# Kernel tuning notes

Measured on AMD Instinct MI355X. Metric: run time of the kernel, lower is better.

The kernel has to match this reference:

```python
import jax, jax.numpy as jnp
import numpy as np

N, E, G = 100_000, 1_600_000, 256
F_IN, H, C = 28, 4, 64
NEG_SLOPE = 0.2
LN_EPS = 1e-5


def _layernorm(x, w, b):
    mu = jnp.mean(x, axis=-1, keepdims=True)
    var = jnp.mean((x - mu) ** 2, axis=-1, keepdims=True)
    return (x - mu) * jax.lax.rsqrt(var + LN_EPS) * w + b


def _gat(x, W, a_src, a_dst, bias, src, dst):
    # PyG GATConv: heads=H, concat=False (mean over heads), add_self_loops=True
    n = x.shape[0]
    loop = jnp.arange(n, dtype=src.dtype)
    s = jnp.concatenate([src, loop])
    d = jnp.concatenate([dst, loop])
    xh = jnp.einsum('nf,hfc->nhc', x, W)              # [N,H,C]
    al_s = jnp.einsum('nhc,hc->nh', xh, a_src)        # [N,H]
    al_d = jnp.einsum('nhc,hc->nh', xh, a_dst)
    e = jax.nn.leaky_relu(al_s[s] + al_d[d], NEG_SLOPE)   # [E',H]
    m = jax.ops.segment_max(e, d, num_segments=n)
    ex = jnp.exp(e - m[d])
    den = jax.ops.segment_sum(ex, d, num_segments=n)
    w = ex / den[d]                                    # scatter-softmax over dst
    out = jax.ops.segment_sum(xh[s] * w[:, :, None], d, num_segments=n)  # [N,H,C]
    return jnp.mean(out, axis=1) + bias


def _gin(x, w1, b1, w2, b2, src, dst):
    # GINConv, eps=0: mlp((1+0)*x + sum_{j->i} x_j)
    agg = jax.ops.segment_sum(x[src], dst, num_segments=x.shape[0])
    h = jax.nn.relu((x + agg) @ w1 + b1)
    return h @ w2 + b2


def _global_attention(x, gw1, gb1, gw2, gb2, batch):
    gate = jax.nn.relu(x @ gw1 + gb1) @ gw2 + gb2      # [N,1]
    m = jax.ops.segment_max(gate, batch, num_segments=G)
    ex = jnp.exp(gate - m[batch])
    den = jax.ops.segment_sum(ex, batch, num_segments=G)
    a = ex / den[batch]
    return jax.ops.segment_sum(a * x, batch, num_segments=G)  # [G,C]


def setup_inputs() -> dict:
    key = jax.random.key(0)
    ks = jax.random.split(key, 32)
    rn = lambda k, shp, s=0.05: (jax.random.normal(k, shp, jnp.float32) * s)
    inp = {
        'x': rn(ks[0], (N, F_IN), 1.0),
        'src': jax.random.randint(ks[1], (E,), 0, N, jnp.int32),
        'dst': jax.random.randint(ks[2], (E,), 0, N, jnp.int32),
        'batch': jnp.sort(jax.random.randint(ks[3], (N,), 0, G, jnp.int32)),
        # GAT layer 1
        'W1': rn(ks[4], (H, F_IN, C)), 'a1s': rn(ks[5], (H, C)), 'a1d': rn(ks[6], (H, C)), 'bg1': jnp.zeros((C,), jnp.float32),
        # GIN mlp1
        'm1w1': rn(ks[7], (C, C)), 'm1b1': jnp.zeros((C,), jnp.float32), 'm1w2': rn(ks[8], (C, C)), 'm1b2': jnp.zeros((C,), jnp.float32),
        'ln1w': jnp.ones((C,), jnp.float32), 'ln1b': jnp.zeros((C,), jnp.float32),
        # GAT layer 2
        'W2': rn(ks[9], (H, C, C)), 'a2s': rn(ks[10], (H, C)), 'a2d': rn(ks[11], (H, C)), 'bg2': jnp.zeros((C,), jnp.float32),
        # GIN mlp2
        'm2w1': rn(ks[12], (C, C)), 'm2b1': jnp.zeros((C,), jnp.float32), 'm2w2': rn(ks[13], (C, C)), 'm2b2': jnp.zeros((C,), jnp.float32),
        'ln2w': jnp.ones((C,), jnp.float32), 'ln2b': jnp.zeros((C,), jnp.float32),
        # gate_nn
        'gw1': rn(ks[14], (C, C)), 'gb1': jnp.zeros((C,), jnp.float32), 'gw2': rn(ks[15], (C, 1)), 'gb2': jnp.zeros((1,), jnp.float32),
        # head
        'l1w': rn(ks[16], (C, 2 * C)), 'l1b': jnp.zeros((2 * C,), jnp.float32),
        'lnfw': jnp.ones((2 * C,), jnp.float32), 'lnfb': jnp.zeros((2 * C,), jnp.float32),
        'l2w': rn(ks[17], (2 * C, 6)), 'l2b': jnp.zeros((6,), jnp.float32),
    }
    return inp


def reference(x, src, dst, batch, W1, a1s, a1d, bg1, m1w1, m1b1, m1w2, m1b2, ln1w, ln1b,
              W2, a2s, a2d, bg2, m2w1, m2b1, m2w2, m2b2, ln2w, ln2b,
              gw1, gb1, gw2, gb2, l1w, l1b, lnfw, lnfb, l2w, l2b):
    # dropout is identity at inference
    xg1 = jax.nn.relu(_gat(x, W1, a1s, a1d, bg1, src, dst))
    x1 = _layernorm(xg1 + _gin(xg1, m1w1, m1b1, m1w2, m1b2, src, dst), ln1w, ln1b)
    xg2 = jax.nn.relu(_gat(x1, W2, a2s, a2d, bg2, src, dst))
    x2 = _layernorm(xg2 + _gin(xg2, m2w1, m2b1, m2w2, m2b2, src, dst), ln2w, ln2b)
    xg = _global_attention(x2, gw1, gb1, gw2, gb2, batch)
    xg = jax.nn.relu(_layernorm(xg @ l1w + l1b, lnfw, lnfb))
    return xg @ l2w + l2b  # [G, 6]
```

## Files before the change

kernel.cpp:

```cpp
#include <hip/hip_runtime.h>

#define N_N 100000
#define N_E 1600000
#define N_G 256
#define F_IN 28
#define HEADS 4
#define CH 64
#define NEG 0.2f
#define LN_EPS 1e-5f

typedef __attribute__((ext_vector_type(8))) short short8v;
typedef __attribute__((ext_vector_type(4))) float float4v;

__device__ __forceinline__ float lrelu(float x) { return x > 0.f ? x : NEG * x; }

__device__ __forceinline__ float wsum(float v) {
#pragma unroll
  for (int o = 32; o > 0; o >>= 1) v += __shfl_xor(v, o, 64);
  return v;
}
__device__ __forceinline__ float wmax(float v) {
#pragma unroll
  for (int o = 32; o > 0; o >>= 1) v = fmaxf(v, __shfl_xor(v, o, 64));
  return v;
}
__device__ __forceinline__ int wsumi(int v) {
#pragma unroll
  for (int o = 32; o > 0; o >>= 1) v += __shfl_xor(v, o, 64);
  return v;
}

__device__ __forceinline__ float bfs(unsigned short u) {
  return __uint_as_float((unsigned)u << 16);
}
__device__ __forceinline__ unsigned short f2bf(float v) {
  unsigned u = __float_as_uint(v);
  return (unsigned short)((u + 0x7fff + ((u >> 16) & 1)) >> 16);
}

__global__ __launch_bounds__(256) void k_deg(const int* __restrict__ dst, int* deg) {
  int e = blockIdx.x * 256 + threadIdx.x;
  if (e < N_E) atomicAdd(&deg[dst[e]], 1);
}

__global__ __launch_bounds__(256) void k_bsum(const int* __restrict__ deg, int* __restrict__ bsum) {
  __shared__ int l[4];
  int t = threadIdx.x;
  int i = blockIdx.x * 256 + t;
  int v = (i < N_N) ? deg[i] : 0;
  int s = wsumi(v);
  if ((t & 63) == 0) l[t >> 6] = s;
  __syncthreads();
  if (t == 0) bsum[blockIdx.x] = l[0] + l[1] + l[2] + l[3];
}

__global__ __launch_bounds__(512) void k_scanb(const int* __restrict__ bsum, int* __restrict__ bofs, int nb) {
  __shared__ int l[512];
  int t = threadIdx.x;
  int v = (t < nb) ? bsum[t] : 0;
  l[t] = v;
  __syncthreads();
  for (int o = 1; o < 512; o <<= 1) {
    int a = (t >= o) ? l[t - o] : 0;
    __syncthreads();
    l[t] += a;
    __syncthreads();
  }
  if (t < nb) bofs[t] = l[t] - v;
}

__global__ __launch_bounds__(256) void k_indptr(const int* __restrict__ deg, const int* __restrict__ bofs,
                                                int* __restrict__ indptr, int* __restrict__ fill) {
  __shared__ int l[256];
  int t = threadIdx.x;
  int i = blockIdx.x * 256 + t;
  int v = (i < N_N) ? deg[i] : 0;
  l[t] = v;
  __syncthreads();
  for (int o = 1; o < 256; o <<= 1) {
    int a = (t >= o) ? l[t - o] : 0;
    __syncthreads();
    l[t] += a;
    __syncthreads();
  }
  if (i < N_N) {
    int p = bofs[blockIdx.x] + l[t] - v;
    indptr[i] = p;
    fill[i] = p;
  }
  if (i == 0) indptr[N_N] = N_E;
}

__global__ __launch_bounds__(256) void k_scatter(const int* __restrict__ src, const int* __restrict__ dst,
                                                 int* fill, int* __restrict__ csr) {
  int e = blockIdx.x * 256 + threadIdx.x;
  if (e < N_E) {
    int d = dst[e];
    int p = atomicAdd(&fill[d], 1);
    csr[p] = src[e];
  }
}

__global__ __launch_bounds__(256) void k_sortw(const int* __restrict__ indptr, int* __restrict__ csr) {
  int wv = threadIdx.x >> 6, lane = threadIdx.x & 63;
  int i = blockIdx.x * 4 + wv;
  if (i >= N_N) return;
  int b = indptr[i], e = indptr[i + 1];
  int deg = e - b;
  if (deg <= 1) return;
  if (deg <= 64) {
    int v = (lane < deg) ? csr[b + lane] : 0x7fffffff;
    int rank = 0;
    for (int j = 0; j < deg; ++j) {
      int vj = __shfl(v, j, 64);
      rank += ((vj < v) || (vj == v && j < lane)) ? 1 : 0;
    }
    if (lane < deg) csr[b + rank] = v;
  } else if (lane == 0) {
    for (int j = b + 1; j < e; ++j) {
      int key = csr[j];
      int k = j - 1;
      while (k >= b && csr[k] > key) { csr[k + 1] = csr[k]; --k; }
      csr[k + 1] = key;
    }
  }
}

__global__ __launch_bounds__(512) void k_gbounds(const int* __restrict__ batch, int* __restrict__ gptr) {
  int g = threadIdx.x;
  if (g > N_G) return;
  int lo = 0, hi = N_N;
  while (lo < hi) {
    int mid = (lo + hi) >> 1;
    if (batch[mid] < g) lo = mid + 1;
    else hi = mid;
  }
  gptr[g] = lo;
}

template <int F>
__global__ __launch_bounds__(256) void k_avec(const float* __restrict__ W, const float* __restrict__ as_,
                                              const float* __restrict__ ad_, float* __restrict__ wsv,
                                              float* __restrict__ wdv) {
  int idx = blockIdx.x * 256 + threadIdx.x;
  if (idx >= HEADS * F) return;
  int h = idx / F, f = idx % F;
  float s = 0.f, d = 0.f;
  for (int c = 0; c < 64; ++c) {
    float w = W[(h * F + f) * 64 + c];
    s = fmaf(w, as_[h * 64 + c], s);
    d = fmaf(w, ad_[h * 64 + c], d);
  }
  wsv[idx] = s;
  wdv[idx] = d;
}

template <int F>
__global__ __launch_bounds__(256) void k_al2(const float* __restrict__ xin, const float* __restrict__ wsv,
                                             const float* __restrict__ wdv, float* __restrict__ al_s,
                                             float* __restrict__ al_d) {
  constexpr int FP = (F % 2 == 0) ? F + 1 : F;
  __shared__ float xl[64][FP];
  __shared__ float wsl[HEADS][F], wdl[HEADS][F];
  int t = threadIdx.x;
  for (int idx = t; idx < HEADS * F; idx += 256) {
    wsl[idx / F][idx % F] = wsv[idx];
    wdl[idx / F][idx % F] = wdv[idx];
  }
  int base = blockIdx.x * 64;
  for (int idx = t; idx < 64 * F; idx += 256) {
    int n = idx / F, f = idx % F;
    int i = base + n;
    xl[n][f] = (i < N_N) ? xin[(size_t)i * F + f] : 0.f;
  }
  __syncthreads();
  int n = t >> 2, h = t & 3;
  int i = base + n;
  if (i < N_N) {
    float s = 0.f, d = 0.f;
#pragma unroll
    for (int f = 0; f < F; ++f) {
      float xv = xl[n][f];
      s = fmaf(xv, wsl[h][f], s);
      d = fmaf(xv, wdl[h][f], d);
    }
    al_s[i * 4 + h] = s;
    al_d[i * 4 + h] = d;
  }
}

template <int F, int NW>
__global__ __launch_bounds__(64 * NW, 4) void k_gat(const float* __restrict__ xin, const int* __restrict__ indptr,
                                                    const int* __restrict__ csr, const float* __restrict__ al_s,
                                                    const float* __restrict__ al_d, const float* __restrict__ W,
                                                    const float* __restrict__ bias, float* __restrict__ xg) {
  constexpr int K = HEADS * F;
  constexpr int KP = (K + 31) & ~31;
  constexpr int KROW = KP + 8;
  __shared__ unsigned short Bt[64][KROW];
  __shared__ unsigned short Ash[16][KROW];
  __shared__ int s_idx[NW][64];
  __shared__ float4 s_w[NW][64];
  int t = threadIdx.x;
  for (int idx = t; idx < K * 64; idx += 64 * NW) {
    int c = idx & 63, hf = idx >> 6;
    Bt[c][hf] = f2bf(W[(size_t)hf * 64 + c]);
  }
  if constexpr (KP > K) {
    for (int idx = t; idx < 64 * (KP - K); idx += 64 * NW)
      Bt[idx / (KP - K)][K + idx % (KP - K)] = 0;
    for (int idx = t; idx < 16 * (KP - K); idx += 64 * NW)
      Ash[idx / (KP - K)][K + idx % (KP - K)] = 0;
  }
  __syncthreads();
  int wv = t >> 6, lane = t & 63;
  int lanef = lane & 31;
  int half = lane >> 5;
  int l15 = lane & 15, g8 = (lane >> 4) * 8;
  float bias_c = (wv < 4) ? bias[16 * wv + l15] : 0.f;
  for (int base = blockIdx.x * 16; base < N_N; base += gridDim.x * 16) {
#pragma unroll
    for (int rep = 0; rep < 2; ++rep) {
      int i = base + wv * 2 + rep;
      if (i < N_N) {
        int b = indptr[i], e = indptr[i + 1];
        float4 ad4 = *(const float4*)&al_d[i * 4];
        float4 as4 = *(const float4*)&al_s[i * 4];
        float ws0 = __expf(lrelu(as4.x + ad4.x));
        float ws1 = __expf(lrelu(as4.y + ad4.y));
        float ws2 = __expf(lrelu(as4.z + ad4.z));
        float ws3 = __expf(lrelu(as4.w + ad4.w));
        float xself = (lane < F) ? xin[(size_t)i * F + lane] : 0.f;
        float a0 = ws0 * xself, a1 = ws1 * xself, a2 = ws2 * xself, a3 = ws3 * xself;
        if (F == F_IN && half) { a0 = 0.f; a1 = 0.f; a2 = 0.f; a3 = 0.f; }
        float pd0 = 0.f, pd1 = 0.f, pd2 = 0.f, pd3 = 0.f;
        for (int cb = b; cb < e; cb += 64) {
          int cnt = min(64, e - cb);
          bool act = (cb + lane) < e;
          int s = 0;
          float w0 = 0.f, w1 = 0.f, w2 = 0.f, w3 = 0.f;
          if (act) {
            s = csr[cb + lane];
            float4 a4 = *(const float4*)&al_s[s * 4];
            w0 = __expf(lrelu(a4.x + ad4.x));
            w1 = __expf(lrelu(a4.y + ad4.y));
            w2 = __expf(lrelu(a4.z + ad4.z));
            w3 = __expf(lrelu(a4.w + ad4.w));
          }
          pd0 += w0; pd1 += w1; pd2 += w2; pd3 += w3;
          s_idx[wv][lane] = s;
          s_w[wv][lane] = make_float4(w0, w1, w2, w3);
          if (F == F_IN) {
            for (int je = 0; je < cnt; je += 16) {
              int sj[8];
#pragma unroll
              for (int u = 0; u < 8; ++u) sj[u] = s_idx[wv][je + 2 * u + half];
              float xr[8];
#pragma unroll
              for (int u = 0; u < 8; ++u)
                xr[u] = (lanef < F_IN) ? xin[(size_t)sj[u] * F_IN + lanef] : 0.f;
#pragma unroll
              for (int u = 0; u < 8; ++u) {
                float4 w4 = s_w[wv][je + 2 * u + half];
                a0 = fmaf(w4.x, xr[u], a0);
                a1 = fmaf(w4.y, xr[u], a1);
                a2 = fmaf(w4.z, xr[u], a2);
                a3 = fmaf(w4.w, xr[u], a3);
              }
            }
          } else {
            for (int je = 0; je < cnt; je += 8) {
              int sj[8];
#pragma unroll
              for (int u = 0; u < 8; ++u) sj[u] = s_idx[wv][je + u];
              float xr[8];
#pragma unroll
              for (int u = 0; u < 8; ++u) xr[u] = xin[(size_t)sj[u] * F + lane];
#pragma unroll
              for (int u = 0; u < 8; ++u) {
                float4 w4 = s_w[wv][je + u];
                a0 = fmaf(w4.x, xr[u], a0);
                a1 = fmaf(w4.y, xr[u], a1);
                a2 = fmaf(w4.z, xr[u], a2);
                a3 = fmaf(w4.w, xr[u], a3);
              }
            }
          }
        }
        if (F == F_IN) {
          a0 += __shfl_xor(a0, 32, 64);
          a1 += __shfl_xor(a1, 32, 64);
          a2 += __shfl_xor(a2, 32, 64);
          a3 += __shfl_xor(a3, 32, 64);
        }
        float dn0 = wsum(pd0) + ws0;
        float dn1 = wsum(pd1) + ws1;
        float dn2 = wsum(pd2) + ws2;
        float dn3 = wsum(pd3) + ws3;
        a0 /= dn0; a1 /= dn1; a2 /= dn2; a3 /= dn3;
        if (lane < F) {
          int n = wv * 2 + rep;
          Ash[n][0 * F + lane] = f2bf(a0);
          Ash[n][1 * F + lane] = f2bf(a1);
          Ash[n][2 * F + lane] = f2bf(a2);
          Ash[n][3 * F + lane] = f2bf(a3);
        }
      }
    }
    __syncthreads();
    if (wv < 4) {
      float4v c4 = {0.f, 0.f, 0.f, 0.f};
#pragma unroll
      for (int kk = 0; kk < KP; kk += 32) {
        short8v af = *(const short8v*)&Ash[l15][kk + g8];
        short8v bf = *(const short8v*)&Bt[16 * wv + l15][kk + g8];
        c4 = __builtin_amdgcn_mfma_f32_16x16x32_bf16(af, bf, c4, 0, 0, 0);
      }
#pragma unroll
      for (int reg = 0; reg < 4; ++reg) {
        int node = base + (g8 >> 1) + reg;
        if (node < N_N) {
          float o = fmaxf(fmaf(c4[reg], 0.25f, bias_c), 0.f);
          xg[(size_t)node * 64 + 16 * wv + l15] = o;
        }
      }
    }
    __syncthreads();
  }
}

template <int NW, bool FUSE_AL, bool FUSE_GATE>
__global__ __launch_bounds__(64 * NW, 4) void k_gin(const int* __restrict__ indptr, const int* __restrict__ csr,
                                                    const float* __restrict__ xg,
                                                    const float* __restrict__ w1,
                                                    const float* __restrict__ b1, const float* __restrict__ w2,
                                                    const float* __restrict__ b2, const float* __restrict__ lnw,
                                                    const float* __restrict__ lnb,
                                                    float* __restrict__ xo,
                                                    const float* __restrict__ wsv, const float* __restrict__ wdv,
                                                    float* __restrict__ al_s, float* __restrict__ al_d,
                                                    const float* __restrict__ gw1, const float* __restrict__ gb1,
                                                    const float* __restrict__ gw2, const float* __restrict__ gb2,
                                                    float* __restrict__ gate) {
  constexpr int KR = 72;
  __shared__ unsigned short W1t[64][KR], W2t[64][KR];
  __shared__ unsigned short GW1t[FUSE_GATE ? 64 : 1][FUSE_GATE ? KR : 1];
  __shared__ unsigned short WVt[FUSE_AL ? 16 : 1][FUSE_AL ? KR : 1];
  __shared__ unsigned short A1h[16][KR], A1l[16][KR], A2s[16][KR];
  __shared__ float A3[16][68];
  __shared__ unsigned short A4[FUSE_GATE ? 16 : 1][FUSE_GATE ? KR : 1];
  __shared__ float gred[4][16];
  int t = threadIdx.x;
  for (int idx = t; idx < 4096; idx += 64 * NW) {
    int k = idx >> 6, c = idx & 63;
    W1t[c][k] = f2bf(w1[idx]);
    W2t[c][k] = f2bf(w2[idx]);
    if constexpr (FUSE_GATE) GW1t[c][k] = f2bf(gw1[idx]);
  }
  if constexpr (FUSE_AL) {
    for (int idx = t; idx < 16 * 64; idx += 64 * NW) {
      int j = idx >> 6, k = idx & 63;
      float v = (j < 4) ? wsv[j * 64 + k] : (j < 8 ? wdv[(j - 4) * 64 + k] : 0.f);
      WVt[j][k] = f2bf(v);
    }
  }
  __syncthreads();
  int wv = t >> 6, lane = t & 63;
  int l15 = lane & 15, g8 = (lane >> 4) * 8;
  float b1c = 0.f, b2c = 0.f, gb1c = 0.f, gw2c = 0.f;
  if (wv < 4) {
    b1c = b1[16 * wv + l15];
    b2c = b2[16 * wv + l15];
    if constexpr (FUSE_GATE) {
      gb1c = gb1[16 * wv + l15];
      gw2c = gw2[16 * wv + l15];
    }
  }
  float lnwv = lnw[lane], lnbv = lnb[lane];
  float gb2v = FUSE_GATE ? gb2[0] : 0.f;
  for (int base = blockIdx.x * 16; base < N_N; base += gridDim.x * 16) {
    float xis[2];
#pragma unroll
    for (int rep = 0; rep < 2; ++rep) {
      int i = base + wv * 2 + rep;
      if (i < N_N) {
        int b = indptr[i], e = indptr[i + 1];
        float xi = xg[(size_t)i * 64 + lane];
        xis[rep] = xi;
        float acc = xi;
        for (int j = b; j < e; j += 8) {
          int cj[8];
#pragma unroll
          for (int u = 0; u < 8; ++u) cj[u] = csr[min(j + u, e - 1)];
          float v[8];
#pragma unroll
          for (int u = 0; u < 8; ++u) v[u] = xg[(size_t)cj[u] * 64 + lane];
#pragma unroll
          for (int u = 0; u < 8; ++u) acc += (j + u) < e ? v[u] : 0.f;
        }
        int n = wv * 2 + rep;
        unsigned short hb = f2bf(acc);
        A1h[n][lane] = hb;
        A1l[n][lane] = f2bf(acc - bfs(hb));
      }
    }
    __syncthreads();
    if (wv < 4) {
      float4v c4 = {0.f, 0.f, 0.f, 0.f};
#pragma unroll
      for (int kk = 0; kk < 64; kk += 32) {
        short8v bf = *(const short8v*)&W1t[16 * wv + l15][kk + g8];
        short8v ah = *(const short8v*)&A1h[l15][kk + g8];
        c4 = __builtin_amdgcn_mfma_f32_16x16x32_bf16(ah, bf, c4, 0, 0, 0);
        short8v al = *(const short8v*)&A1l[l15][kk + g8];
        c4 = __builtin_amdgcn_mfma_f32_16x16x32_bf16(al, bf, c4, 0, 0, 0);
      }
#pragma unroll
      for (int reg = 0; reg < 4; ++reg)
        A2s[(g8 >> 1) + reg][16 * wv + l15] = f2bf(fmaxf(c4[reg] + b1c, 0.f));
    }
    __syncthreads();
    if (wv < 4) {
      float4v c4 = {0.f, 0.f, 0.f, 0.f};
#pragma unroll
      for (int kk = 0; kk < 64; kk += 32) {
        short8v af = *(const short8v*)&A2s[l15][kk + g8];
        short8v bf = *(const short8v*)&W2t[16 * wv + l15][kk + g8];
        c4 = __builtin_amdgcn_mfma_f32_16x16x32_bf16(af, bf, c4, 0, 0, 0);
      }
#pragma unroll
      for (int reg = 0; reg < 4; ++reg) A3[(g8 >> 1) + reg][16 * wv + l15] = c4[reg] + b2c;
    }
    __syncthreads();
#pragma unroll
    for (int rep = 0; rep < 2; ++rep) {
      int i = base + wv * 2 + rep;
      if (i < N_N) {
        int n = wv * 2 + rep;
        float res = xis[rep] + A3[n][lane];
        float mu = wsum(res) * (1.f / 64.f);
        float d = res - mu;
        float var = wsum(d * d) * (1.f / 64.f);
        float xov = fmaf(d * rsqrtf(var + LN_EPS), lnwv, lnbv);
        xo[(size_t)i * 64 + lane] = xov;
        if constexpr (FUSE_AL) {
          unsigned short hb = f2bf(xov);
          A1h[n][lane] = hb;
          A1l[n][lane] = f2bf(xov - bfs(hb));
        }
        if constexpr (FUSE_GATE) A4[n][lane] = f2bf(xov);
      }
    }
    if constexpr (FUSE_AL) {
      __syncthreads();
      if (wv == 0) {
        float4v c4 = {0.f, 0.f, 0.f, 0.f};
#pragma unroll
        for (int kk = 0; kk < 64; kk += 32) {
          short8v bf = *(const short8v*)&WVt[l15][kk + g8];
          short8v ah = *(const short8v*)&A1h[l15][kk + g8];
          c4 = __builtin_amdgcn_mfma_f32_16x16x32_bf16(ah, bf, c4, 0, 0, 0);
          short8v al = *(const short8v*)&A1l[l15][kk + g8];
          c4 = __builtin_amdgcn_mfma_f32_16x16x32_bf16(al, bf, c4, 0, 0, 0);
        }
#pragma unroll
        for (int reg = 0; reg < 4; ++reg) {
          int node = base + (g8 >> 1) + reg;
          if (node < N_N) {
            if (l15 < 4) al_s[node * 4 + l15] = c4[reg];
            else if (l15 < 8) al_d[node * 4 + (l15 - 4)] = c4[reg];
          }
        }
      }
      __syncthreads();
    }
    if constexpr (FUSE_GATE) {
      __syncthreads();
      if (wv < 4) {
        float4v c4 = {0.f, 0.f, 0.f, 0.f};
#pragma unroll
        for (int kk = 0; kk < 64; kk += 32) {
          short8v af = *(const short8v*)&A4[l15][kk + g8];
          short8v bf = *(const short8v*)&GW1t[16 * wv + l15][kk + g8];
          c4 = __builtin_amdgcn_mfma_f32_16x16x32_bf16(af, bf, c4, 0, 0, 0);
        }
#pragma unroll
        for (int reg = 0; reg < 4; ++reg) {
          float m = fmaxf(c4[reg] + gb1c, 0.f) * gw2c;
          m += __shfl_xor(m, 1, 64);
          m += __shfl_xor(m, 2, 64);
          m += __shfl_xor(m, 4, 64);
          m += __shfl_xor(m, 8, 64);
          if (l15 == 0) gred[wv][(g8 >> 1) + reg] = m;
        }
      }
      __syncthreads();
      if (wv == 0 && lane < 16) {
        int node = base + lane;
        if (node < N_N)
          gate[node] = gred[0][lane] + gred[1][lane] + gred[2][lane] + gred[3][lane] + gb2v;
      }
      __syncthreads();
    }
  }
}

__global__ __launch_bounds__(256) void k_pool(const int* __restrict__ gptr, const float* __restrict__ gate,
                                              const float* __restrict__ x2, float* __restrict__ pooled) {
  int g = blockIdx.x;
  int t = threadIdx.x, wv = t >> 6, lane = t & 63;
  __shared__ float red[256];
  int b = gptr[g], e = gptr[g + 1];
  if (b == e) {
    if (t < 64) pooled[g * 64 + t] = 0.f;
    return;
  }
  float m = -1e30f;
  for (int j = b + t; j < e; j += 256) m = fmaxf(m, gate[j]);
  m = wmax(m);
  if (lane == 0) red[wv] = m;
  __syncthreads();
  m = fmaxf(fmaxf(red[0], red[1]), fmaxf(red[2], red[3]));
  __syncthreads();
  float dn = 0.f;
  for (int j = b + t; j < e; j += 256) dn += __expf(gate[j] - m);
  dn = wsum(dn);
  if (lane == 0) red[wv] = dn;
  __syncthreads();
  dn = red[0] + red[1] + red[2] + red[3];
  __syncthreads();
  float acc = 0.f;
  for (int j = b + wv; j < e; j += 4) acc = fmaf(__expf(gate[j] - m), x2[(size_t)j * 64 + lane], acc);
  red[t] = acc;
  __syncthreads();
  if (t < 64) pooled[g * 64 + t] = (red[t] + red[t + 64] + red[t + 128] + red[t + 192]) / dn;
}

__global__ __launch_bounds__(128) void k_head(const float* __restrict__ pooled, const float* __restrict__ l1w,
                                              const float* __restrict__ l1b, const float* __restrict__ lnfw,
                                              const float* __restrict__ lnfb, const float* __restrict__ l2w,
                                              const float* __restrict__ l2b, float* __restrict__ out) {
  int g = blockIdx.x, t = threadIdx.x;
  __shared__ float pl[64], zl[128], red[2];
  if (t < 64) pl[t] = pooled[g * 64 + t];
  __syncthreads();
  float y = l1b[t];
#pragma unroll 8
  for (int k = 0; k < 64; ++k) y = fmaf(pl[k], l1w[k * 128 + t], y);
  int wv = t >> 6, lane = t & 63;
  float s = wsum(y);
  if (lane == 0) red[wv] = s;
  __syncthreads();
  float mu = (red[0] + red[1]) * (1.f / 128.f);
  float d = y - mu;
  __syncthreads();
  s = wsum(d * d);
  if (lane == 0) red[wv] = s;
  __syncthreads();
  float var = (red[0] + red[1]) * (1.f / 128.f);
  float z = fmaxf(fmaf(d * rsqrtf(var + LN_EPS), lnfw[t], lnfb[t]), 0.f);
  zl[t] = z;
  __syncthreads();
  if (t < 6) {
    float o = l2b[t];
    for (int k = 0; k < 128; ++k) o = fmaf(zl[k], l2w[k * 6 + t], o);
    out[g * 6 + t] = o;
  }
}

extern "C" void kernel_launch(void* const* d_in, const int* in_sizes, int n_in,
                              void* d_out, int out_size, void* d_ws, size_t ws_size,
                              hipStream_t stream) {
  const float* x = (const float*)d_in[0];
  const int* src = (const int*)d_in[1];
  const int* dst = (const int*)d_in[2];
  const int* batch = (const int*)d_in[3];
  const float* W1 = (const float*)d_in[4];
  const float* a1s = (const float*)d_in[5];
  const float* a1d = (const float*)d_in[6];
  const float* bg1 = (const float*)d_in[7];
  const float* m1w1 = (const float*)d_in[8];
  const float* m1b1 = (const float*)d_in[9];
  const float* m1w2 = (const float*)d_in[10];
  const float* m1b2 = (const float*)d_in[11];
  const float* ln1w = (const float*)d_in[12];
  const float* ln1b = (const float*)d_in[13];
  const float* W2 = (const float*)d_in[14];
  const float* a2s = (const float*)d_in[15];
  const float* a2d = (const float*)d_in[16];
  const float* bg2 = (const float*)d_in[17];
  const float* m2w1 = (const float*)d_in[18];
  const float* m2b1 = (const float*)d_in[19];
  const float* m2w2 = (const float*)d_in[20];
  const float* m2b2 = (const float*)d_in[21];
  const float* ln2w = (const float*)d_in[22];
  const float* ln2b = (const float*)d_in[23];
  const float* gw1 = (const float*)d_in[24];
  const float* gb1 = (const float*)d_in[25];
  const float* gw2 = (const float*)d_in[26];
  const float* gb2 = (const float*)d_in[27];
  const float* l1w = (const float*)d_in[28];
  const float* l1b = (const float*)d_in[29];
  const float* lnfw = (const float*)d_in[30];
  const float* lnfb = (const float*)d_in[31];
  const float* l2w = (const float*)d_in[32];
  const float* l2b = (const float*)d_in[33];
  float* out = (float*)d_out;

  char* ws = (char*)d_ws;
  size_t off = 0;
  auto alloc = [&](size_t bytes) -> void* {
    void* p = ws + off;
    off += (bytes + 255) & ~(size_t)255;
    return p;
  };
  int* indptr = (int*)alloc((N_N + 1) * sizeof(int));
  int* fill = (int*)alloc(N_N * sizeof(int));
  int* csr = (int*)alloc((size_t)N_E * sizeof(int));
  int* bsum = (int*)alloc(512 * sizeof(int));
  int* bofs = (int*)alloc(512 * sizeof(int));
  int* gptr = (int*)alloc(257 * sizeof(int));
  float* wsv = (float*)alloc(HEADS * 64 * sizeof(float));
  float* wdv = (float*)alloc(HEADS * 64 * sizeof(float));
  float* al_s = (float*)alloc((size_t)N_N * 4 * sizeof(float));
  float* al_d = (float*)alloc((size_t)N_N * 4 * sizeof(float));
  float* gate = (float*)alloc((size_t)N_N * sizeof(float));
  float* pooled = (float*)alloc(N_G * 64 * sizeof(float));
  float* xg = (float*)alloc((size_t)N_N * 64 * sizeof(float));
  float* xv = (float*)alloc((size_t)N_N * 64 * sizeof(float));
  (void)ws_size; (void)n_in; (void)in_sizes; (void)out_size;

  const int NBE = (N_E + 255) / 256;
  const int NBN = (N_N + 255) / 256;

  hipMemsetAsync(fill, 0, (size_t)N_N * sizeof(int), stream);
  k_deg<<<NBE, 256, 0, stream>>>(dst, fill);
  k_bsum<<<NBN, 256, 0, stream>>>(fill, bsum);
  k_scanb<<<1, 512, 0, stream>>>(bsum, bofs, NBN);
  k_indptr<<<NBN, 256, 0, stream>>>(fill, bofs, indptr, fill);
  k_scatter<<<NBE, 256, 0, stream>>>(src, dst, fill, csr);
  k_sortw<<<(N_N + 3) / 4, 256, 0, stream>>>(indptr, csr);
  k_gbounds<<<1, 512, 0, stream>>>(batch, gptr);

  k_avec<F_IN><<<1, 256, 0, stream>>>(W1, a1s, a1d, wsv, wdv);
  k_al2<F_IN><<<(N_N + 63) / 64, 256, 0, stream>>>(x, wsv, wdv, al_s, al_d);
  k_gat<F_IN, 8><<<2048, 512, 0, stream>>>(x, indptr, csr, al_s, al_d, W1, bg1, xg);
  k_avec<CH><<<1, 256, 0, stream>>>(W2, a2s, a2d, wsv, wdv);
  k_gin<8, true, false><<<2048, 512, 0, stream>>>(indptr, csr, xg, m1w1, m1b1, m1w2, m1b2, ln1w, ln1b,
                                                  xv, wsv, wdv, al_s, al_d, gw1, gb1, gw2, gb2, gate);
  k_gat<CH, 8><<<2048, 512, 0, stream>>>(xv, indptr, csr, al_s, al_d, W2, bg2, xg);
  k_gin<8, false, true><<<2048, 512, 0, stream>>>(indptr, csr, xg, m2w1, m2b1, m2w2, m2b2, ln2w, ln2b,
                                                  xv, wsv, wdv, al_s, al_d, gw1, gb1, gw2, gb2, gate);
  k_pool<<<N_G, 256, 0, stream>>>(gptr, gate, xv, pooled);
  k_head<<<N_G, 128, 0, stream>>>(pooled, l1w, l1b, lnfw, lnfb, l2w, l2b, out);
}
```

Baseline: 719.6 us.

## Build CSR via two-level bucketed sort using shared-memory histograms

New measurement: 622.4 us. 13.5% less time.

```diff
diff --git a/kernel.cpp b/kernel.cpp
--- a/kernel.cpp
+++ b/kernel.cpp
@@ -8,6 +8,8 @@
 #define CH 64
 #define NEG 0.2f
 #define LN_EPS 1e-5f
+#define NBKT 391
+#define BCAP 6144
 
 typedef __attribute__((ext_vector_type(8))) short short8v;
 typedef __attribute__((ext_vector_type(4))) float float4v;
@@ -22,11 +24,6 @@
 __device__ __forceinline__ float wmax(float v) {
 #pragma unroll
   for (int o = 32; o > 0; o >>= 1) v = fmaxf(v, __shfl_xor(v, o, 64));
-  return v;
-}
-__device__ __forceinline__ int wsumi(int v) {
-#pragma unroll
-  for (int o = 32; o > 0; o >>= 1) v += __shfl_xor(v, o, 64);
   return v;
 }
 
@@ -38,26 +35,25 @@
   return (unsigned short)((u + 0x7fff + ((u >> 16) & 1)) >> 16);
 }
 
-__global__ __launch_bounds__(256) void k_deg(const int* __restrict__ dst, int* deg) {
-  int e = blockIdx.x * 256 + threadIdx.x;
-  if (e < N_E) atomicAdd(&deg[dst[e]], 1);
-}
-
-__global__ __launch_bounds__(256) void k_bsum(const int* __restrict__ deg, int* __restrict__ bsum) {
-  __shared__ int l[4];
+
+__global__ __launch_bounds__(256) void k_ccount(const int* __restrict__ dst, int* __restrict__ ccnt) {
+  __shared__ int h[NBKT];
   int t = threadIdx.x;
-  int i = blockIdx.x * 256 + t;
-  int v = (i < N_N) ? deg[i] : 0;
-  int s = wsumi(v);
-  if ((t & 63) == 0) l[t >> 6] = s;
-  __syncthreads();
-  if (t == 0) bsum[blockIdx.x] = l[0] + l[1] + l[2] + l[3];
-}
-
-__global__ __launch_bounds__(512) void k_scanb(const int* __restrict__ bsum, int* __restrict__ bofs, int nb) {
+  for (int i = t; i < NBKT; i += 256) h[i] = 0;
+  __syncthreads();
+  int base = blockIdx.x * 4096;
+  int cnt = min(4096, N_E - base);
+  for (int j = t; j < cnt; j += 256) atomicAdd(&h[dst[base + j] >> 8], 1);
+  __syncthreads();
+  for (int i = t; i < NBKT; i += 256)
+    if (h[i]) atomicAdd(&ccnt[i], h[i]);
+}
+
+__global__ __launch_bounds__(512) void k_cscan(const int* __restrict__ ccnt, int* __restrict__ cbase,
+                                               int* __restrict__ cfill) {
   __shared__ int l[512];
   int t = threadIdx.x;
-  int v = (t < nb) ? bsum[t] : 0;
+  int v = (t < NBKT) ? ccnt[t] : 0;
   l[t] = v;
   __syncthreads();
   for (int o = 1; o < 512; o <<= 1) {
@@ -66,62 +62,142 @@
     l[t] += a;
     __syncthreads();
   }
-  if (t < nb) bofs[t] = l[t] - v;
-}
-
-__global__ __launch_bounds__(256) void k_indptr(const int* __restrict__ deg, const int* __restrict__ bofs,
-                                                int* __restrict__ indptr, int* __restrict__ fill) {
-  __shared__ int l[256];
+  if (t < NBKT) {
+    cbase[t] = l[t] - v;
+    cfill[t] = l[t] - v;
+  }
+}
+
+__global__ __launch_bounds__(256) void k_cscat(const int* __restrict__ src, const int* __restrict__ dst,
+                                               int* cfill, unsigned long long* __restrict__ pairs) {
+  __shared__ unsigned long long pl[4096];
+  __shared__ unsigned long long outp[4096];
+  __shared__ int h[NBKT], sc[NBKT], gpos[NBKT], f2[NBKT];
   int t = threadIdx.x;
-  int i = blockIdx.x * 256 + t;
-  int v = (i < N_N) ? deg[i] : 0;
-  l[t] = v;
-  __syncthreads();
-  for (int o = 1; o < 256; o <<= 1) {
-    int a = (t >= o) ? l[t - o] : 0;
-    __syncthreads();
-    l[t] += a;
-    __syncthreads();
-  }
-  if (i < N_N) {
-    int p = bofs[blockIdx.x] + l[t] - v;
-    indptr[i] = p;
-    fill[i] = p;
-  }
-  if (i == 0) indptr[N_N] = N_E;
-}
-
-__global__ __launch_bounds__(256) void k_scatter(const int* __restrict__ src, const int* __restrict__ dst,
-                                                 int* fill, int* __restrict__ csr) {
-  int e = blockIdx.x * 256 + threadIdx.x;
-  if (e < N_E) {
-    int d = dst[e];
-    int p = atomicAdd(&fill[d], 1);
-    csr[p] = src[e];
-  }
-}
-
-__global__ __launch_bounds__(256) void k_sortw(const int* __restrict__ indptr, int* __restrict__ csr) {
-  int wv = threadIdx.x >> 6, lane = threadIdx.x & 63;
-  int i = blockIdx.x * 4 + wv;
-  if (i >= N_N) return;
-  int b = indptr[i], e = indptr[i + 1];
-  int deg = e - b;
-  if (deg <= 1) return;
-  if (deg <= 64) {
-    int v = (lane < deg) ? csr[b + lane] : 0x7fffffff;
-    int rank = 0;
-    for (int j = 0; j < deg; ++j) {
-      int vj = __shfl(v, j, 64);
-      rank += ((vj < v) || (vj == v && j < lane)) ? 1 : 0;
-    }
-    if (lane < deg) csr[b + rank] = v;
-  } else if (lane == 0) {
-    for (int j = b + 1; j < e; ++j) {
-      int key = csr[j];
-      int k = j - 1;
-      while (k >= b && csr[k] > key) { csr[k + 1] = csr[k]; --k; }
-      csr[k + 1] = key;
+  for (int i = t; i < NBKT; i += 256) {
+    h[i] = 0;
+    f2[i] = 0;
+  }
+  __syncthreads();
+  int base = blockIdx.x * 4096;
+  int cnt = min(4096, N_E - base);
+  for (int j = t; j < cnt; j += 256) {
+    int d = dst[base + j];
+    pl[j] = ((unsigned long long)(unsigned)d << 32) | (unsigned)src[base + j];
+    atomicAdd(&h[d >> 8], 1);
+  }
+  __syncthreads();
+  for (int i = t; i < NBKT; i += 256) sc[i] = h[i];
+  __syncthreads();
+  for (int o = 1; o < NBKT; o <<= 1) {
+    int v0 = 0, v1 = 0;
+    int i2 = t + 256;
+    if (t >= o) v0 = sc[t - o];
+    if (i2 < NBKT && i2 >= o) v1 = sc[i2 - o];
+    __syncthreads();
+    if (t >= o) sc[t] += v0;
+    if (i2 < NBKT && i2 >= o) sc[i2] += v1;
+    __syncthreads();
+  }
+  for (int i = t; i < NBKT; i += 256)
+    if (h[i]) gpos[i] = atomicAdd(&cfill[i], h[i]);
+  __syncthreads();
+  for (int j = t; j < cnt; j += 256) {
+    unsigned long long p = pl[j];
+    int bin = (int)(p >> 40);
+    int r = atomicAdd(&f2[bin], 1);
+    outp[sc[bin] - h[bin] + r] = p;
+  }
+  __syncthreads();
+  for (int j = t; j < cnt; j += 256) {
+    unsigned long long p = outp[j];
+    int bin = (int)(p >> 40);
+    pairs[gpos[bin] + (j - (sc[bin] - h[bin]))] = p;
+  }
+}
+
+__global__ __launch_bounds__(256) void k_build(const int* __restrict__ ccnt, const int* __restrict__ cbase,
+                                               const unsigned long long* __restrict__ pairs,
+                                               int* __restrict__ indptr, int* __restrict__ csr) {
+  __shared__ unsigned long long pl[BCAP];
+  __shared__ int sl[BCAP];
+  __shared__ int degl[256], lofs[256], fil[256];
+  int nb = blockIdx.x, t = threadIdx.x;
+  int gbase = cbase[nb], cnt = ccnt[nb];
+  int nn = min(256, N_N - nb * 256);
+  if (t == 0 && nb == 0) indptr[N_N] = N_E;
+  if (cnt <= BCAP) {
+    for (int j = t; j < cnt; j += 256) pl[j] = pairs[gbase + j];
+    degl[t] = 0;
+    __syncthreads();
+    for (int j = t; j < cnt; j += 256) atomicAdd(&degl[(int)((pl[j] >> 32) & 255)], 1);
+    __syncthreads();
+    int v = degl[t];
+    lofs[t] = v;
+    __syncthreads();
+    for (int o = 1; o < 256; o <<= 1) {
+      int a = (t >= o) ? lofs[t - o] : 0;
+      __syncthreads();
+      lofs[t] += a;
+      __syncthreads();
+    }
+    int excl = lofs[t] - v;
+    if (t < nn) indptr[nb * 256 + t] = gbase + excl;
+    fil[t] = excl;
+    __syncthreads();
+    for (int j = t; j < cnt; j += 256) {
+      unsigned long long p = pl[j];
+      int node = (int)((p >> 32) & 255);
+      int pos = atomicAdd(&fil[node], 1);
+      sl[pos] = (int)(unsigned)p;
+    }
+    __syncthreads();
+    int wv = t >> 6, lane = t & 63;
+    for (int q = wv; q < 256; q += 4) {
+      int d = degl[q];
+      if (d <= 1) continue;
+      int b = lofs[q] - d;
+      if (d <= 64) {
+        int vv = (lane < d) ? sl[b + lane] : 0x7fffffff;
+        int rank = 0;
+        for (int j2 = 0; j2 < d; ++j2) {
+          int vj = __shfl(vv, j2, 64);
+          rank += ((vj < vv) || (vj == vv && j2 < lane)) ? 1 : 0;
+        }
+        if (lane < d) sl[b + rank] = vv;
+      } else if (lane == 0) {
+        for (int j2 = b + 1; j2 < b + d; ++j2) {
+          int key = sl[j2];
+          int k2 = j2 - 1;
+          while (k2 >= b && sl[k2] > key) { sl[k2 + 1] = sl[k2]; --k2; }
+          sl[k2 + 1] = key;
+        }
+      }
+    }
+    __syncthreads();
+    for (int j = t; j < cnt; j += 256) csr[gbase + j] = sl[j];
+  } else if (t == 0) {
+    for (int n = 0; n < nn; ++n) degl[n] = 0;
+    for (int j = 0; j < cnt; ++j) degl[(int)((pairs[gbase + j] >> 32) & 255)]++;
+    int run = 0;
+    for (int n = 0; n < nn; ++n) {
+      indptr[nb * 256 + n] = gbase + run;
+      fil[n] = run;
+      run += degl[n];
+    }
+    for (int j = 0; j < cnt; ++j) {
+      unsigned long long p = pairs[gbase + j];
+      int node = (int)((p >> 32) & 255);
+      csr[gbase + fil[node]++] = (int)(unsigned)p;
+    }
+    for (int n = 0; n < nn; ++n) {
+      int b = indptr[nb * 256 + n], e2 = b + degl[n];
+      for (int j2 = b + 1; j2 < e2; ++j2) {
+        int key = csr[j2];
+        int k2 = j2 - 1;
+        while (k2 >= b && csr[k2] > key) { csr[k2 + 1] = csr[k2]; --k2; }
+        csr[k2 + 1] = key;
+      }
     }
   }
 }
@@ -615,10 +691,11 @@
     return p;
   };
   int* indptr = (int*)alloc((N_N + 1) * sizeof(int));
-  int* fill = (int*)alloc(N_N * sizeof(int));
   int* csr = (int*)alloc((size_t)N_E * sizeof(int));
-  int* bsum = (int*)alloc(512 * sizeof(int));
-  int* bofs = (int*)alloc(512 * sizeof(int));
+  unsigned long long* pairs = (unsigned long long*)alloc((size_t)N_E * sizeof(unsigned long long));
+  int* ccnt = (int*)alloc(NBKT * sizeof(int));
+  int* cbase = (int*)alloc(NBKT * sizeof(int));
+  int* cfill = (int*)alloc(NBKT * sizeof(int));
   int* gptr = (int*)alloc(257 * sizeof(int));
   float* wsv = (float*)alloc(HEADS * 64 * sizeof(float));
   float* wdv = (float*)alloc(HEADS * 64 * sizeof(float));
@@ -630,16 +707,13 @@
   float* xv = (float*)alloc((size_t)N_N * 64 * sizeof(float));
   (void)ws_size; (void)n_in; (void)in_sizes; (void)out_size;
 
-  const int NBE = (N_E + 255) / 256;
-  const int NBN = (N_N + 255) / 256;
-
-  hipMemsetAsync(fill, 0, (size_t)N_N * sizeof(int), stream);
-  k_deg<<<NBE, 256, 0, stream>>>(dst, fill);
-  k_bsum<<<NBN, 256, 0, stream>>>(fill, bsum);
-  k_scanb<<<1, 512, 0, stream>>>(bsum, bofs, NBN);
-  k_indptr<<<NBN, 256, 0, stream>>>(fill, bofs, indptr, fill);
-  k_scatter<<<NBE, 256, 0, stream>>>(src, dst, fill, csr);
-  k_sortw<<<(N_N + 3) / 4, 256, 0, stream>>>(indptr, csr);
+  const int NCB = (N_E + 4095) / 4096;
+
+  hipMemsetAsync(ccnt, 0, NBKT * sizeof(int), stream);
+  k_ccount<<<NCB, 256, 0, stream>>>(dst, ccnt);
+  k_cscan<<<1, 512, 0, stream>>>(ccnt, cbase, cfill);
+  k_cscat<<<NCB, 256, 0, stream>>>(src, dst, cfill, pairs);
+  k_build<<<NBKT, 256, 0, stream>>>(ccnt, cbase, pairs, indptr, csr);
   k_gbounds<<<1, 512, 0, stream>>>(batch, gptr);
 
   k_avec<F_IN><<<1, 256, 0, stream>>>(W1, a1s, a1d, wsv, wdv);
```
